# Performance work log

Measured on AMD Instinct MI355X. Metric: run time of the kernel, lower is better.

Reference implementation:

```python
import jax, jax.numpy as jnp
import numpy as np

DECAY = 0.99
EPSILON = 1e-05


def setup_inputs() -> dict:
    key = jax.random.key(0)
    k1, k2, k3, k4 = jax.random.split(key, 4)
    B, S, D, K = 16, 2048, 512, 2048
    x = jax.random.normal(k1, (B, S, D), dtype=jnp.float32)
    embed = jax.random.normal(k2, (K, D), dtype=jnp.float32)
    cluster_size = jax.random.uniform(k3, (K,), dtype=jnp.float32)
    embed_avg = jax.random.normal(k4, (K, D), dtype=jnp.float32)
    return {"x": x, "embed": embed, "cluster_size": cluster_size, "embed_avg": embed_avg}


def reference(x, embed, cluster_size, embed_avg):
    # x: [B,S,D]  embed: [K,D]  cluster_size: [K]  embed_avg: [K,D]
    B, S, D = x.shape
    K = embed.shape[0]
    xf = x.reshape(-1, D)  # [N,D], N=B*S

    # quantize(): negative squared euclidean distance, argmax over codebook
    x_sq = jnp.sum(xf * xf, axis=1, keepdims=True)            # [N,1]
    e_sq = jnp.sum(embed * embed, axis=1)[None, :]            # [1,K]
    dist = -(x_sq - 2.0 * (xf @ embed.T) + e_sq)              # [N,K]
    embed_ind = jnp.argmax(dist, axis=-1)                     # [N] int

    # dequantize
    quantize = embed[embed_ind].reshape(B, S, D)

    # training EMA updates (onehot.sum(0) and x^T @ onehot expressed as segment sums)
    ones = jnp.ones((xf.shape[0],), dtype=x.dtype)
    bins = jax.ops.segment_sum(ones, embed_ind, num_segments=K)        # [K] == onehot.sum(0)
    embed_sum_t = jax.ops.segment_sum(xf, embed_ind, num_segments=K)   # [K,D] == (x.T @ onehot).T

    new_cluster_size = cluster_size * DECAY + (1.0 - DECAY) * bins
    new_embed_avg = embed_avg * DECAY + (1.0 - DECAY) * embed_sum_t

    total = new_cluster_size.sum()
    smoothed = (new_cluster_size + EPSILON) / (total + K * EPSILON) * total  # laplace smoothing
    new_embed = new_embed_avg / smoothed[:, None]

    return (quantize,
            embed_ind.reshape(B, S),
            dist.reshape(B, S, K),
            new_cluster_size,
            new_embed_avg,
            new_embed)
```

## Files before the change

### kernel.cpp

```cpp
#include <hip/hip_runtime.h>

#define DECAY 0.99f
#define OMD   0.01f
#define EPS   1e-5f

constexpr int Bb = 16, Ss = 2048, Dd = 512, Kk = 2048;
constexpr int Nn = Bb * Ss;

typedef __attribute__((ext_vector_type(8))) short short8;
typedef __attribute__((ext_vector_type(4))) float f32x4;

__device__ __forceinline__ unsigned short f2bf(float x) {
    unsigned u = __float_as_uint(x);
    unsigned r = (u + 0x7FFFu + ((u >> 16) & 1u)) >> 16;
    return (unsigned short)r;
}
__device__ __forceinline__ float bf2f(unsigned short u) {
    return __uint_as_float((unsigned)u << 16);
}

__device__ __forceinline__ void gload_lds16(const void* g, void* l) {
    __builtin_amdgcn_global_load_lds(
        (const __attribute__((address_space(1))) void*)g,
        (__attribute__((address_space(3))) void*)l, 16, 0, 0);
}

#define BARRIER() do { asm volatile("" ::: "memory"); \
                       __builtin_amdgcn_s_barrier();  \
                       asm volatile("" ::: "memory"); } while (0)

__global__ void rows_sq(const float* __restrict__ in, float* __restrict__ out, int nrows) {
    int row  = blockIdx.x * 4 + (threadIdx.x >> 6);
    int lane = threadIdx.x & 63;
    if (row >= nrows) return;
    const float4* p = (const float4*)(in + (size_t)row * Dd);
    float s = 0.f;
    #pragma unroll
    for (int i = 0; i < 2; ++i) {
        float4 v = p[lane + 64 * i];
        s += v.x * v.x + v.y * v.y + v.z * v.z + v.w * v.w;
    }
    #pragma unroll
    for (int off = 32; off; off >>= 1) s += __shfl_down(s, off);
    if (lane == 0) out[row] = s;
}

__global__ void conv_split(const float* __restrict__ in,
                           unsigned short* __restrict__ ph,
                           unsigned short* __restrict__ pm,
                           unsigned short* __restrict__ pl, int n4) {
    int i = blockIdx.x * 256 + threadIdx.x;
    if (i >= n4) return;
    float4 v = ((const float4*)in)[i];
    float f[4] = {v.x, v.y, v.z, v.w};
    ushort4 h, m, l;
    unsigned short hh[4], mm[4], ll[4];
    #pragma unroll
    for (int j = 0; j < 4; ++j) {
        float x = f[j];
        unsigned short a = f2bf(x);  float ra = x - bf2f(a);
        unsigned short b = f2bf(ra); float rb = ra - bf2f(b);
        unsigned short c = f2bf(rb);
        hh[j] = a; mm[j] = b; ll[j] = c;
    }
    h.x = hh[0]; h.y = hh[1]; h.z = hh[2]; h.w = hh[3];
    m.x = mm[0]; m.y = mm[1]; m.z = mm[2]; m.w = mm[3];
    l.x = ll[0]; l.y = ll[1]; l.z = ll[2]; l.w = ll[3];
    ((ushort4*)ph)[i] = h;
    ((ushort4*)pm)[i] = m;
    ((ushort4*)pl)[i] = l;
}

__global__ __launch_bounds__(512, 1) void gemm_split256(
    const unsigned short* __restrict__ xp,
    const unsigned short* __restrict__ ep,
    const float* __restrict__ xsq,
    const float* __restrict__ esq,
    float* __restrict__ dist,
    unsigned long long* __restrict__ packed)
{
    __shared__ unsigned short As[2][256][64];
    __shared__ unsigned short Bs[2][256][64];

    const int tid  = threadIdx.x;
    const int lane = tid & 63;
    const int wid  = tid >> 6;
    const int wr   = wid >> 2;
    const int wc   = wid & 3;

    int bid = blockIdx.x;
    int wg  = (bid & 7) * 128 + (bid >> 3);
    int mb  = wg >> 3, nb = wg & 7;
    const int row0 = mb * 256, col0 = nb * 256;

    f32x4 acc[8][4] = {};
    short8 af[4], afh[4], bf[2], bfh[2];

    const int l8   = lane >> 3;
    const int csrc = (lane & 7) ^ l8;

    auto stageAt = [&](const unsigned short* pl, int d, int tt) {
        int ko = (tt & 7) * 64;
        #pragma unroll
        for (int jj = 0; jj < 4; ++jj) {
            int rowbase = jj * 64 + wid * 8;
            const unsigned short* src =
                pl + (size_t)(row0 + rowbase + l8) * Dd + ko + csrc * 8;
            gload_lds16(src, &As[d][rowbase][0]);
        }
    };
    auto stageBt = [&](const unsigned short* pl, int d, int tt) {
        int ko = (tt & 7) * 64;
        #pragma unroll
        for (int jj = 0; jj < 4; ++jj) {
            int rowbase = jj * 64 + wid * 8;
            const unsigned short* src =
                pl + (size_t)(col0 + rowbase + l8) * Dd + ko + csrc * 8;
            gload_lds16(src, &Bs[d][rowbase][0]);
        }
    };

    auto readA4 = [&](int d, int msel) {
        #pragma unroll
        for (int m = 0; m < 4; ++m) {
            int r  = wr * 128 + (msel * 4 + m) * 16 + (lane & 15);
            int c  = ((lane >> 4))     ^ (r & 7);
            int c2 = ((lane >> 4) + 4) ^ (r & 7);
            af[m]  = *(const short8*)&As[d][r][c * 8];
            afh[m] = *(const short8*)&As[d][r][c2 * 8];
        }
    };
    auto readB2 = [&](int d, int nsel) {
        #pragma unroll
        for (int n = 0; n < 2; ++n) {
            int r  = wc * 64 + (nsel * 2 + n) * 16 + (lane & 15);
            int c  = ((lane >> 4))     ^ (r & 7);
            int c2 = ((lane >> 4) + 4) ^ (r & 7);
            bf[n]  = *(const short8*)&Bs[d][r][c * 8];
            bfh[n] = *(const short8*)&Bs[d][r][c2 * 8];
        }
    };

    auto mfmaQ = [&](int msel, int nsel) {
        __builtin_amdgcn_s_setprio(1);
        #pragma unroll
        for (int m = 0; m < 4; ++m)
            #pragma unroll
            for (int n = 0; n < 2; ++n) {
                int am = msel * 4 + m, bn = nsel * 2 + n;
                acc[am][bn] = __builtin_amdgcn_mfma_f32_16x16x32_bf16(af[m], bf[n], acc[am][bn], 0, 0, 0);
            }
        #pragma unroll
        for (int m = 0; m < 4; ++m)
            #pragma unroll
            for (int n = 0; n < 2; ++n) {
                int am = msel * 4 + m, bn = nsel * 2 + n;
                acc[am][bn] = __builtin_amdgcn_mfma_f32_16x16x32_bf16(afh[m], bfh[n], acc[am][bn], 0, 0, 0);
            }
        __builtin_amdgcn_s_setprio(0);
    };

    stageAt(xp, 0, 0);
    stageBt(ep, 0, 0);
    asm volatile("s_waitcnt vmcnt(0)" ::: "memory");
    BARRIER();

    for (int t = 0; t < 32; ++t) {
        const int cur = t & 1, nxt = cur ^ 1;
        const bool st = (t < 31);
        int pn = (t + 1) >> 3;
        const unsigned short* Apn = xp + (size_t)((pn == 2 || pn == 3) ? 1 : 0) * ((size_t)Nn * Dd);
        const unsigned short* Bpn = ep + (size_t)((pn == 1 || pn == 3) ? 1 : 0) * ((size_t)Kk * Dd);

        readA4(cur, 0); readB2(cur, 0);
        if (st) { stageAt(Apn, nxt, t + 1); stageBt(Bpn, nxt, t + 1); }
        mfmaQ(0, 0);
        BARRIER();
        readB2(cur, 1);
        mfmaQ(0, 1);
        BARRIER();
        readA4(cur, 1);
        mfmaQ(1, 1);
        BARRIER();
        readB2(cur, 0);
        mfmaQ(1, 0);
        asm volatile("s_waitcnt vmcnt(0)" ::: "memory");
        BARRIER();
    }

    const int jrow = (lane >> 4) * 4;
    const int ncol = lane & 15;
    #pragma unroll
    for (int m = 0; m < 8; ++m) {
        int rbase = row0 + wr * 128 + m * 16 + jrow;
        #pragma unroll
        for (int j = 0; j < 4; ++j) {
            int row = rbase + j;
            float xs = xsq[row];
            float best = -3.4e38f; int bi = 0;
            #pragma unroll
            for (int n = 0; n < 4; ++n) {
                int col = col0 + wc * 64 + n * 16 + ncol;
                float v = 2.f * acc[m][n][j] - xs - esq[col];
                dist[(size_t)row * Kk + col] = v;
                if (v > best) { best = v; bi = col; }
            }
            unsigned u = __float_as_uint(best);
            u = (u & 0x80000000u) ? ~u : (u | 0x80000000u);
            unsigned long long pk = ((unsigned long long)u << 32) | (unsigned)(~bi);
            #pragma unroll
            for (int off = 1; off < 16; off <<= 1) {
                unsigned long long o = __shfl_xor(pk, off);
                if (o > pk) pk = o;
            }
            if (ncol == 0) atomicMax(&packed[row], pk);
        }
    }
}

__global__ void unpack_argmax(const unsigned long long* __restrict__ packed,
                              float* __restrict__ ind_f, int* __restrict__ ind_i) {
    int i = blockIdx.x * 256 + threadIdx.x;
    unsigned long long p = packed[i];
    int k = (int)(~(unsigned)(p & 0xFFFFFFFFull));
    ind_f[i] = (float)k;
    ind_i[i] = k;
}

#define BM 64
#define BN 64
#define BK 32
__global__ __launch_bounds__(256) void gemm_dist(
    const float* __restrict__ A, const float* __restrict__ Bm,
    const float* __restrict__ xsq, const float* __restrict__ esq,
    float* __restrict__ dist)
{
    __shared__ float Asl[BK][BM + 4];
    __shared__ float Bsl[BK][BN + 4];
    int tid = threadIdx.x;
    int row0 = blockIdx.x * BM, col0 = blockIdx.y * BN;
    int tx = tid & 15, ty = tid >> 4;
    float acc[4][4] = {};
    int lr = tid >> 3, lc = (tid & 7) * 4;
    for (int d0 = 0; d0 < Dd; d0 += BK) {
        float4 a0 = *(const float4*)(A  + (size_t)(row0 + lr)      * Dd + d0 + lc);
        float4 a1 = *(const float4*)(A  + (size_t)(row0 + lr + 32) * Dd + d0 + lc);
        float4 b0 = *(const float4*)(Bm + (size_t)(col0 + lr)      * Dd + d0 + lc);
        float4 b1 = *(const float4*)(Bm + (size_t)(col0 + lr + 32) * Dd + d0 + lc);
        __syncthreads();
        Asl[lc + 0][lr] = a0.x; Asl[lc + 1][lr] = a0.y; Asl[lc + 2][lr] = a0.z; Asl[lc + 3][lr] = a0.w;
        Asl[lc + 0][lr + 32] = a1.x; Asl[lc + 1][lr + 32] = a1.y; Asl[lc + 2][lr + 32] = a1.z; Asl[lc + 3][lr + 32] = a1.w;
        Bsl[lc + 0][lr] = b0.x; Bsl[lc + 1][lr] = b0.y; Bsl[lc + 2][lr] = b0.z; Bsl[lc + 3][lr] = b0.w;
        Bsl[lc + 0][lr + 32] = b1.x; Bsl[lc + 1][lr + 32] = b1.y; Bsl[lc + 2][lr + 32] = b1.z; Bsl[lc + 3][lr + 32] = b1.w;
        __syncthreads();
        #pragma unroll
        for (int kd = 0; kd < BK; ++kd) {
            float4 av = *(const float4*)&Asl[kd][ty * 4];
            float4 bv = *(const float4*)&Bsl[kd][tx * 4];
            float a[4] = {av.x, av.y, av.z, av.w};
            float b[4] = {bv.x, bv.y, bv.z, bv.w};
            #pragma unroll
            for (int i = 0; i < 4; ++i)
                #pragma unroll
                for (int j = 0; j < 4; ++j)
                    acc[i][j] = fmaf(a[i], b[j], acc[i][j]);
        }
    }
    #pragma unroll
    for (int i = 0; i < 4; ++i) {
        int row = row0 + ty * 4 + i;
        float xs = xsq[row];
        float4 o;
        int col = col0 + tx * 4;
        o.x = 2.f * acc[i][0] - xs - esq[col + 0];
        o.y = 2.f * acc[i][1] - xs - esq[col + 1];
        o.z = 2.f * acc[i][2] - xs - esq[col + 2];
        o.w = 2.f * acc[i][3] - xs - esq[col + 3];
        *(float4*)(dist + (size_t)row * Kk + col) = o;
    }
}

__global__ void argmax_k(const float* __restrict__ dist,
                         float* __restrict__ ind_f, int* __restrict__ ind_i) {
    int row  = blockIdx.x * 4 + (threadIdx.x >> 6);
    int lane = threadIdx.x & 63;
    const float4* p = (const float4*)(dist + (size_t)row * Kk);
    float best = -3.4e38f;
    int bidx = 0;
    #pragma unroll
    for (int it = 0; it < Kk / 4 / 64; ++it) {
        int i = lane + it * 64;
        float4 v = p[i];
        int base = i * 4;
        if (v.x > best) { best = v.x; bidx = base + 0; }
        if (v.y > best) { best = v.y; bidx = base + 1; }
        if (v.z > best) { best = v.z; bidx = base + 2; }
        if (v.w > best) { best = v.w; bidx = base + 3; }
    }
    #pragma unroll
    for (int off = 32; off; off >>= 1) {
        float ov = __shfl_down(best, off);
        int   oi = __shfl_down(bidx, off);
        if (ov > best || (ov == best && oi < bidx)) { best = ov; bidx = oi; }
    }
    if (lane == 0) { ind_f[row] = (float)bidx; ind_i[row] = bidx; }
}

__global__ void gather_scatter(const float* __restrict__ x,
                               const float* __restrict__ embed,
                               const int* __restrict__ ind,
                               float* __restrict__ quant,
                               float* __restrict__ esum,
                               int* __restrict__ bins) {
    int n = blockIdx.x;
    int k = ind[n];
    int t = threadIdx.x;
    size_t xb = (size_t)n * Dd;
    size_t eb = (size_t)k * Dd;
    float v0 = x[xb + t];
    float v1 = x[xb + t + 256];
    quant[xb + t]       = embed[eb + t];
    quant[xb + t + 256] = embed[eb + t + 256];
    atomicAdd(&esum[eb + t],       v0);
    atomicAdd(&esum[eb + t + 256], v1);
    if (t == 0) atomicAdd(&bins[k], 1);
}

__global__ void finalize1(const float* __restrict__ cs, const int* __restrict__ bins,
                          float* __restrict__ ncs, float* __restrict__ total_ws) {
    __shared__ float red[16];
    int t = threadIdx.x;
    float s = 0.f;
    for (int k = t; k < Kk; k += 1024) {
        float v = cs[k] * DECAY + OMD * (float)bins[k];
        ncs[k] = v;
        s += v;
    }
    #pragma unroll
    for (int off = 32; off; off >>= 1) s += __shfl_down(s, off);
    if ((t & 63) == 0) red[t >> 6] = s;
    __syncthreads();
    if (t == 0) {
        float tot = 0.f;
        #pragma unroll
        for (int i = 0; i < 16; ++i) tot += red[i];
        total_ws[0] = tot;
    }
}

__global__ void finalize2(const float* __restrict__ ea, const float* __restrict__ esum,
                          const float* __restrict__ ncs, const float* __restrict__ total_ws,
                          float* __restrict__ nea, float* __restrict__ ne) {
    int idx = blockIdx.x * 256 + threadIdx.x;
    float total = total_ws[0];
    int k = idx >> 7;
    float sm = (ncs[k] + EPS) / (total + Kk * EPS) * total;
    float inv = 1.f / sm;
    float4 a = ((const float4*)ea)[idx];
    float4 s = ((const float4*)esum)[idx];
    float4 r;
    r.x = a.x * DECAY + OMD * s.x;
    r.y = a.y * DECAY + OMD * s.y;
    r.z = a.z * DECAY + OMD * s.z;
    r.w = a.w * DECAY + OMD * s.w;
    ((float4*)nea)[idx] = r;
    float4 e;
    e.x = r.x * inv; e.y = r.y * inv; e.z = r.z * inv; e.w = r.w * inv;
    ((float4*)ne)[idx] = e;
}

extern "C" void kernel_launch(void* const* d_in, const int* in_sizes, int n_in,
                              void* d_out, int out_size, void* d_ws, size_t ws_size,
                              hipStream_t stream) {
    const float* x     = (const float*)d_in[0];
    const float* embed = (const float*)d_in[1];
    const float* cs    = (const float*)d_in[2];
    const float* ea    = (const float*)d_in[3];

    float* out     = (float*)d_out;
    float* o_quant = out;
    float* o_ind   = o_quant + (size_t)Nn * Dd;
    float* o_dist  = o_ind + Nn;
    float* o_ncs   = o_dist + (size_t)Nn * Kk;
    float* o_nea   = o_ncs + Kk;
    float* o_ne    = o_nea + (size_t)Kk * Dd;

    size_t xp_elems = (size_t)3 * Nn * Dd;
    size_t ep_elems = (size_t)3 * Kk * Dd;
    char* w = (char*)d_ws;
    unsigned short* xp = (unsigned short*)w;                 w += xp_elems * 2;
    unsigned short* epp = (unsigned short*)w;                w += ep_elems * 2;
    float* xsq   = (float*)w;                                w += (size_t)Nn * 4;
    float* esq   = (float*)w;                                w += (size_t)Kk * 4;
    int*   ind_i = (int*)w;                                  w += (size_t)Nn * 4;
    int*   bins  = (int*)w;                                  w += (size_t)Kk * 4;
    float* esum  = (float*)w;                                w += (size_t)Kk * Dd * 4;
    unsigned long long* packed = (unsigned long long*)w;     w += (size_t)Nn * 8;
    float* total = (float*)w;                                w += 256;
    size_t need = (size_t)(w - (char*)d_ws);

    if (ws_size >= need) {
        hipMemsetAsync(bins, 0, (size_t)Kk * 4 + (size_t)Kk * Dd * 4 + (size_t)Nn * 8, stream);

        rows_sq<<<Nn / 4, 256, 0, stream>>>(x, xsq, Nn);
        rows_sq<<<Kk / 4, 256, 0, stream>>>(embed, esq, Kk);

        conv_split<<<(Nn * Dd / 4 + 255) / 256, 256, 0, stream>>>(
            x, xp, xp + (size_t)Nn * Dd, xp + (size_t)2 * Nn * Dd, Nn * Dd / 4);
        conv_split<<<(Kk * Dd / 4 + 255) / 256, 256, 0, stream>>>(
            embed, epp, epp + (size_t)Kk * Dd, epp + (size_t)2 * Kk * Dd, Kk * Dd / 4);

        gemm_split256<<<(Nn / 256) * (Kk / 256), 512, 0, stream>>>(
            xp, epp, xsq, esq, o_dist, packed);

        unpack_argmax<<<Nn / 256, 256, 0, stream>>>(packed, o_ind, ind_i);
    } else {
        float* fxsq  = (float*)d_ws;
        float* fesq  = fxsq + Nn;
        int*   find  = (int*)(fesq + Kk);
        int*   fbins = find + Nn;
        float* fesum = (float*)(fbins + Kk);
        float* ftot  = fesum + (size_t)Kk * Dd;
        xsq = fxsq; esq = fesq; ind_i = find; bins = fbins; esum = fesum; total = ftot;

        hipMemsetAsync(bins, 0, (size_t)(Kk + Kk * Dd) * sizeof(float), stream);
        rows_sq<<<Nn / 4, 256, 0, stream>>>(x, xsq, Nn);
        rows_sq<<<Kk / 4, 256, 0, stream>>>(embed, esq, Kk);
        dim3 g(Nn / BM, Kk / BN);
        gemm_dist<<<g, 256, 0, stream>>>(x, embed, xsq, esq, o_dist);
        argmax_k<<<Nn / 4, 256, 0, stream>>>(o_dist, o_ind, ind_i);
    }

    gather_scatter<<<Nn, 256, 0, stream>>>(x, embed, ind_i, o_quant, esum, bins);
    finalize1<<<1, 1024, 0, stream>>>(cs, bins, o_ncs, total);
    finalize2<<<(Kk * Dd / 4) / 256, 256, 0, stream>>>(ea, esum, o_ncs, total, o_nea, o_ne);
}
```

Baseline: 456.7 us.

## Drop third bf16 split plane and remove intra-tile barriers in GEMM loop

The conversion kernel now produces only the high and mid bf16 pieces of each float instead of three, which cuts conversion writes and workspace traffic. The GEMM main loop loads both halves of the B fragment up front into separate registers, so the three barriers between the quarter MFMA groups go away. The s_setprio hints around the MFMA groups are also removed. This adds register pressure, and dropping the low plane was not used by the GEMM anyway, but it changes the preprocessing cost.

```diff
diff --git a/kernel.cpp b/kernel.cpp
--- a/kernel.cpp
+++ b/kernel.cpp
@@ -45,30 +45,26 @@
     if (lane == 0) out[row] = s;
 }
 
-__global__ void conv_split(const float* __restrict__ in,
-                           unsigned short* __restrict__ ph,
-                           unsigned short* __restrict__ pm,
-                           unsigned short* __restrict__ pl, int n4) {
+__global__ void conv_split2(const float* __restrict__ in,
+                            unsigned short* __restrict__ ph,
+                            unsigned short* __restrict__ pm, int n4) {
     int i = blockIdx.x * 256 + threadIdx.x;
     if (i >= n4) return;
     float4 v = ((const float4*)in)[i];
     float f[4] = {v.x, v.y, v.z, v.w};
-    ushort4 h, m, l;
-    unsigned short hh[4], mm[4], ll[4];
+    ushort4 h, m;
+    unsigned short hh[4], mm[4];
     #pragma unroll
     for (int j = 0; j < 4; ++j) {
         float x = f[j];
         unsigned short a = f2bf(x);  float ra = x - bf2f(a);
-        unsigned short b = f2bf(ra); float rb = ra - bf2f(b);
-        unsigned short c = f2bf(rb);
-        hh[j] = a; mm[j] = b; ll[j] = c;
+        unsigned short b = f2bf(ra);
+        hh[j] = a; mm[j] = b;
     }
     h.x = hh[0]; h.y = hh[1]; h.z = hh[2]; h.w = hh[3];
     m.x = mm[0]; m.y = mm[1]; m.z = mm[2]; m.w = mm[3];
-    l.x = ll[0]; l.y = ll[1]; l.z = ll[2]; l.w = ll[3];
     ((ushort4*)ph)[i] = h;
     ((ushort4*)pm)[i] = m;
-    ((ushort4*)pl)[i] = l;
 }
 
 __global__ __launch_bounds__(512, 1) void gemm_split256(
@@ -94,7 +90,7 @@
     const int row0 = mb * 256, col0 = nb * 256;
 
     f32x4 acc[8][4] = {};
-    short8 af[4], afh[4], bf[2], bfh[2];
+    short8 af[4], afh[4], bl[2], blh[2], bh[2], bhh[2];
 
     const int l8   = lane >> 3;
     const int csrc = (lane & 7) ^ l8;
@@ -130,34 +126,42 @@
             afh[m] = *(const short8*)&As[d][r][c2 * 8];
         }
     };
-    auto readB2 = [&](int d, int nsel) {
+    auto readBlo = [&](int d) {
         #pragma unroll
         for (int n = 0; n < 2; ++n) {
-            int r  = wc * 64 + (nsel * 2 + n) * 16 + (lane & 15);
+            int r  = wc * 64 + n * 16 + (lane & 15);
             int c  = ((lane >> 4))     ^ (r & 7);
             int c2 = ((lane >> 4) + 4) ^ (r & 7);
-            bf[n]  = *(const short8*)&Bs[d][r][c * 8];
-            bfh[n] = *(const short8*)&Bs[d][r][c2 * 8];
-        }
-    };
-
-    auto mfmaQ = [&](int msel, int nsel) {
-        __builtin_amdgcn_s_setprio(1);
+            bl[n]  = *(const short8*)&Bs[d][r][c * 8];
+            blh[n] = *(const short8*)&Bs[d][r][c2 * 8];
+        }
+    };
+    auto readBhi = [&](int d) {
+        #pragma unroll
+        for (int n = 0; n < 2; ++n) {
+            int r  = wc * 64 + (2 + n) * 16 + (lane & 15);
+            int c  = ((lane >> 4))     ^ (r & 7);
+            int c2 = ((lane >> 4) + 4) ^ (r & 7);
+            bh[n]  = *(const short8*)&Bs[d][r][c * 8];
+            bhh[n] = *(const short8*)&Bs[d][r][c2 * 8];
+        }
+    };
+
+    auto mfmaQ = [&](int msel, int nsel, const short8* b0, const short8* b1) {
         #pragma unroll
         for (int m = 0; m < 4; ++m)
             #pragma unroll
             for (int n = 0; n < 2; ++n) {
                 int am = msel * 4 + m, bn = nsel * 2 + n;
-                acc[am][bn] = __builtin_amdgcn_mfma_f32_16x16x32_bf16(af[m], bf[n], acc[am][bn], 0, 0, 0);
+                acc[am][bn] = __builtin_amdgcn_mfma_f32_16x16x32_bf16(af[m], b0[n], acc[am][bn], 0, 0, 0);
             }
         #pragma unroll
         for (int m = 0; m < 4; ++m)
             #pragma unroll
             for (int n = 0; n < 2; ++n) {
                 int am = msel * 4 + m, bn = nsel * 2 + n;
-                acc[am][bn] = __builtin_amdgcn_mfma_f32_16x16x32_bf16(afh[m], bfh[n], acc[am][bn], 0, 0, 0);
+                acc[am][bn] = __builtin_amdgcn_mfma_f32_16x16x32_bf16(afh[m], b1[n], acc[am][bn], 0, 0, 0);
             }
-        __builtin_amdgcn_s_setprio(0);
     };
 
     stageAt(xp, 0, 0);
@@ -172,18 +176,13 @@
         const unsigned short* Apn = xp + (size_t)((pn == 2 || pn == 3) ? 1 : 0) * ((size_t)Nn * Dd);
         const unsigned short* Bpn = ep + (size_t)((pn == 1 || pn == 3) ? 1 : 0) * ((size_t)Kk * Dd);
 
-        readA4(cur, 0); readB2(cur, 0);
+        readA4(cur, 0); readBlo(cur); readBhi(cur);
         if (st) { stageAt(Apn, nxt, t + 1); stageBt(Bpn, nxt, t + 1); }
-        mfmaQ(0, 0);
-        BARRIER();
-        readB2(cur, 1);
-        mfmaQ(0, 1);
-        BARRIER();
+        mfmaQ(0, 0, bl, blh);
+        mfmaQ(0, 1, bh, bhh);
         readA4(cur, 1);
-        mfmaQ(1, 1);
-        BARRIER();
-        readB2(cur, 0);
-        mfmaQ(1, 0);
+        mfmaQ(1, 1, bh, bhh);
+        mfmaQ(1, 0, bl, blh);
         asm volatile("s_waitcnt vmcnt(0)" ::: "memory");
         BARRIER();
     }
@@ -405,10 +404,10 @@
         rows_sq<<<Nn / 4, 256, 0, stream>>>(x, xsq, Nn);
         rows_sq<<<Kk / 4, 256, 0, stream>>>(embed, esq, Kk);
 
-        conv_split<<<(Nn * Dd / 4 + 255) / 256, 256, 0, stream>>>(
-            x, xp, xp + (size_t)Nn * Dd, xp + (size_t)2 * Nn * Dd, Nn * Dd / 4);
-        conv_split<<<(Kk * Dd / 4 + 255) / 256, 256, 0, stream>>>(
-            embed, epp, epp + (size_t)Kk * Dd, epp + (size_t)2 * Kk * Dd, Kk * Dd / 4);
+        conv_split2<<<(Nn * Dd / 4 + 255) / 256, 256, 0, stream>>>(
+            x, xp, xp + (size_t)Nn * Dd, Nn * Dd / 4);
+        conv_split2<<<(Kk * Dd / 4 + 255) / 256, 256, 0, stream>>>(
+            embed, epp, epp + (size_t)Kk * Dd, Kk * Dd / 4);
 
         gemm_split256<<<(Nn / 256) * (Kk / 256), 512, 0, stream>>>(
             xp, epp, xsq, esq, o_dist, packed);
```

New measurement: 440.8 us. -3.5%, faster.
